# Kernel optimization log

Measured on AMD Instinct MI355X. Metric: run time of the kernel, lower is better.

## Reference

```python
import jax, jax.numpy as jnp
import numpy as np

D_IN, D_OUT, RANK = 4096, 4096, 16
ALPHA = 1.0


def setup_inputs() -> dict:
    key = jax.random.key(0)
    ks = jax.random.split(key, 7)
    x = jax.random.normal(ks[0], (8, 2048, D_IN), dtype=jnp.float32)
    W = jax.random.normal(ks[1], (D_IN, D_OUT), dtype=jnp.float32) * (1.0 / np.sqrt(D_IN))
    bias = jax.random.normal(ks[2], (D_OUT,), dtype=jnp.float32) * 0.02
    # he_normal init for a factors; b factors are zeros in the layer, but use small
    # random values so the adapter path contributes numerically to the test.
    a0 = jax.random.normal(ks[3], (D_IN, RANK), dtype=jnp.float32) * np.sqrt(2.0 / D_IN)
    b0 = jax.random.normal(ks[4], (RANK, D_OUT), dtype=jnp.float32) * 0.02
    a1 = jax.random.normal(ks[5], (D_IN, RANK), dtype=jnp.float32) * np.sqrt(2.0 / D_IN)
    b1 = jax.random.normal(ks[6], (RANK, D_OUT), dtype=jnp.float32) * 0.02
    return {"x": x, "W": W, "bias": bias, "a0": a0, "b0": b0, "a1": a1, "b1": b1}


def reference(x, W, bias, a0, b0, a1, b1):
    # LoHA kernel: base + Hadamard product of scaled low-rank factors
    scale = ALPHA / RANK
    p0 = scale * (a0 @ b0)            # [d_in, d_out]
    p1 = scale * (a1 @ b1)            # [d_in, d_out]
    kernel = W + p0 * p1              # [d_in, d_out]
    # Dense call: x @ kernel + bias
    return jnp.einsum('bsd,de->bse', x, kernel) + bias
```

## Files before the change

kernel.cpp:

```cpp
#include <hip/hip_runtime.h>


#define D_IN   4096
#define D_OUT  4096
#define RANKR  16
#define MROWS  16384
#define NTK    128

typedef __attribute__((ext_vector_type(8))) short short8;
typedef __attribute__((ext_vector_type(4))) float floatx4;

__device__ __forceinline__ unsigned short f2bf(float f) {
    union { float f; unsigned u; } c; c.f = f;
    unsigned r = c.u + 0x7fffu + ((c.u >> 16) & 1u);
    return (unsigned short)(r >> 16);
}

__device__ __forceinline__ void glds16(const void* g, void* l) {
    __builtin_amdgcn_global_load_lds(
        (const __attribute__((address_space(1))) void*)g,
        (__attribute__((address_space(3))) void*)l, 16, 0, 0);
}

__global__ __launch_bounds__(256) void cvt_x(const float* __restrict__ x,
                                             unsigned short* __restrict__ xb) {
    size_t i = ((size_t)blockIdx.x * 256 + threadIdx.x) * 8;
    const float4* p = (const float4*)(x + i);
    float4 v0 = p[0], v1 = p[1];
    union { unsigned short u[8]; uint4 q; } o;
    o.u[0] = f2bf(v0.x); o.u[1] = f2bf(v0.y);
    o.u[2] = f2bf(v0.z); o.u[3] = f2bf(v0.w);
    o.u[4] = f2bf(v1.x); o.u[5] = f2bf(v1.y);
    o.u[6] = f2bf(v1.z); o.u[7] = f2bf(v1.w);
    *(uint4*)(xb + i) = o.q;
}

__global__ __launch_bounds__(256) void prep_bt(
    const float* __restrict__ W,  const float* __restrict__ a0,
    const float* __restrict__ b0, const float* __restrict__ a1,
    const float* __restrict__ b1, unsigned short* __restrict__ Bt) {
    __shared__ float Wt[64][65];
    __shared__ float b0t[64][20], b1t[64][20];
    const int tid = threadIdx.x;
    const int k0 = (blockIdx.x & 63) * 64, n0 = (blockIdx.x >> 6) * 64;

    #pragma unroll
    for (int i = 0; i < 16; ++i) {
        int e = i * 256 + tid;
        int kk = e >> 6, nn = e & 63;
        Wt[kk][nn] = W[(size_t)(k0 + kk) * D_OUT + n0 + nn];
    }
    #pragma unroll
    for (int i = 0; i < 4; ++i) {
        int e = i * 256 + tid;
        int r = e >> 6, nn = e & 63;
        b0t[nn][r] = b0[(size_t)r * D_OUT + n0 + nn];
        b1t[nn][r] = b1[(size_t)r * D_OUT + n0 + nn];
    }
    const int kk = tid & 63;
    float4 A0[4], A1[4];
    #pragma unroll
    for (int c = 0; c < 4; ++c) {
        A0[c] = *(const float4*)(a0 + (size_t)(k0 + kk) * RANKR + c * 4);
        A1[c] = *(const float4*)(a1 + (size_t)(k0 + kk) * RANKR + c * 4);
    }
    __syncthreads();

    const float s2 = 1.0f / 256.0f;
    #pragma unroll
    for (int i = 0; i < 16; ++i) {
        int nn = i * 4 + (tid >> 6);
        float d0 = 0.f, d1 = 0.f;
        #pragma unroll
        for (int c = 0; c < 4; ++c) {
            float4 bv0 = *(const float4*)&b0t[nn][c * 4];
            float4 bv1 = *(const float4*)&b1t[nn][c * 4];
            d0 += A0[c].x * bv0.x + A0[c].y * bv0.y + A0[c].z * bv0.z + A0[c].w * bv0.w;
            d1 += A1[c].x * bv1.x + A1[c].y * bv1.y + A1[c].z * bv1.z + A1[c].w * bv1.w;
        }
        float v = Wt[kk][nn] + s2 * d0 * d1;
        Bt[(size_t)(n0 + nn) * D_IN + k0 + kk] = f2bf(v);
    }
}

#define STAGE_A(tt) do {                                                      \
    const int kt_ = (tt) * 32;                                                \
    unsigned short* const dst_ = &As[(tt) & 3][0];                            \
    _Pragma("unroll")                                                         \
    for (int r_ = 0; r_ < 2; ++r_) {                                          \
      const int e_ = r_ * 512 + tid;                                          \
      const int row_ = e_ >> 2;                                               \
      const int cc_ = ((e_ & 3) ^ ((row_ >> 2) & 3)) * 8;                     \
      glds16(Ag + (size_t)row_ * D_IN + kt_ + cc_,                            \
             (char*)dst_ + r_ * 8192 + wave * 1024);                          \
    }                                                                         \
  } while (0)

#define STAGE_B(tt) do {                                                      \
    const int kt_ = (tt) * 32;                                                \
    unsigned short* const dst_ = &Bs[(tt) & 3][0];                            \
    _Pragma("unroll")                                                         \
    for (int r_ = 0; r_ < 2; ++r_) {                                          \
      const int e_ = r_ * 512 + tid;                                          \
      const int row_ = e_ >> 2;                                               \
      const int cc_ = ((e_ & 3) ^ ((row_ >> 2) & 3)) * 8;                     \
      glds16(Bg + (size_t)row_ * D_IN + kt_ + cc_,                            \
             (char*)dst_ + r_ * 8192 + wave * 1024);                          \
    }                                                                         \
  } while (0)

#define TILE(tt, DS) do {                                                     \
    const unsigned short* const as_ = &As[(tt) & 3][0];                       \
    const unsigned short* const bs_ = &Bs[(tt) & 3][0];                       \
    if (DS) STAGE_A((tt) + 3);                                                \
    short8 bfr[4], afr[4];                                                    \
    _Pragma("unroll")                                                         \
    for (int nt_ = 0; nt_ < 4; ++nt_)                                         \
      bfr[nt_] = *(const short8*)(bs_ + (wn * 64 + nt_ * 16 + l16) * 32 + rc8); \
    _Pragma("unroll")                                                         \
    for (int mt_ = 0; mt_ < 4; ++mt_)                                         \
      afr[mt_] = *(const short8*)(as_ + (wm * 128 + mt_ * 16 + l16) * 32 + rc8); \
    __builtin_amdgcn_s_setprio(1);                                            \
    _Pragma("unroll")                                                         \
    for (int mt_ = 0; mt_ < 4; ++mt_)                                         \
      _Pragma("unroll")                                                       \
      for (int nt_ = 0; nt_ < 4; ++nt_)                                       \
        acc[mt_][nt_] = __builtin_amdgcn_mfma_f32_16x16x32_bf16(              \
            afr[mt_], bfr[nt_], acc[mt_][nt_], 0, 0, 0);                      \
    __builtin_amdgcn_s_setprio(0);                                            \
    if (DS) STAGE_B((tt) + 3);                                                \
    _Pragma("unroll")                                                         \
    for (int mt_ = 0; mt_ < 4; ++mt_)                                         \
      afr[mt_] = *(const short8*)(as_ + (wm * 128 + 64 + mt_ * 16 + l16) * 32 + rc8); \
    __builtin_amdgcn_s_setprio(1);                                            \
    _Pragma("unroll")                                                         \
    for (int mt_ = 0; mt_ < 4; ++mt_)                                         \
      _Pragma("unroll")                                                       \
      for (int nt_ = 0; nt_ < 4; ++nt_)                                       \
        acc[4 + mt_][nt_] = __builtin_amdgcn_mfma_f32_16x16x32_bf16(          \
            afr[mt_], bfr[nt_], acc[4 + mt_][nt_], 0, 0, 0);                  \
    __builtin_amdgcn_s_setprio(0);                                            \
  } while (0)

#define TILE_SYNC(N) do {                                                     \
    asm volatile("s_waitcnt vmcnt(" #N ")" ::: "memory");                     \
    __builtin_amdgcn_s_barrier();                                             \
    asm volatile("" ::: "memory");                                            \
  } while (0)

__global__ __launch_bounds__(512, 2) void gemm_bt(
    const unsigned short* __restrict__ A,
    const unsigned short* __restrict__ B,
    const float* __restrict__ bias,
    float* __restrict__ C) {
    __shared__ __align__(16) unsigned short As[4][256 * 32];
    __shared__ __align__(16) unsigned short Bs[4][256 * 32];

    const int tid  = threadIdx.x;
    const int wave = tid >> 6, lane = tid & 63;
    const int quad = lane >> 4, l16 = lane & 15;
    const int rc8  = (quad ^ (l16 >> 2)) * 8;

    const int bid = blockIdx.y * 16 + blockIdx.x;
    const int swz = (bid & 7) * 128 + (bid >> 3);
    const int m0 = (swz >> 4) * 256, n0 = (swz & 15) * 256;
    const int wm = wave >> 2, wn = wave & 3;

    const unsigned short* Ag = A + (size_t)m0 * D_IN;
    const unsigned short* Bg = B + (size_t)n0 * D_IN;

    floatx4 acc[8][4] = {};

    STAGE_A(0); STAGE_B(0);
    STAGE_A(1); STAGE_B(1);
    STAGE_A(2); STAGE_B(2);
    TILE_SYNC(8);

    for (int t = 0; t < NTK - 3; ++t) {
        TILE(t, 1);
        TILE_SYNC(8);
    }
    TILE(NTK - 3, 0); TILE_SYNC(4);
    TILE(NTK - 2, 0); TILE_SYNC(0);
    TILE(NTK - 1, 0);

    #pragma unroll
    for (int nt = 0; nt < 4; ++nt) {
        int col = n0 + wn * 64 + nt * 16 + l16;
        float bv = bias[col];
        #pragma unroll
        for (int mt = 0; mt < 8; ++mt) {
            int r0 = m0 + wm * 128 + mt * 16 + quad * 4;
            #pragma unroll
            for (int r = 0; r < 4; ++r) {
                float v = acc[mt][nt][r] + bv;
                __builtin_nontemporal_store(v, &C[(size_t)(r0 + r) * D_OUT + col]);
            }
        }
    }
}

extern "C" void kernel_launch(void* const* d_in, const int* in_sizes, int n_in,
                              void* d_out, int out_size, void* d_ws, size_t ws_size,
                              hipStream_t stream) {
    const float* x    = (const float*)d_in[0];
    const float* W    = (const float*)d_in[1];
    const float* bias = (const float*)d_in[2];
    const float* a0   = (const float*)d_in[3];
    const float* b0   = (const float*)d_in[4];
    const float* a1   = (const float*)d_in[5];
    const float* b1   = (const float*)d_in[6];
    float* out = (float*)d_out;

    unsigned short* xb = (unsigned short*)d_ws;
    unsigned short* Bt = (unsigned short*)((char*)d_ws + (size_t)MROWS * D_IN * 2);

    cvt_x<<<(MROWS * (size_t)D_IN) / 2048, 256, 0, stream>>>(x, xb);
    prep_bt<<<4096, 256, 0, stream>>>(W, a0, b0, a1, b1, Bt);
    gemm_bt<<<dim3(D_OUT / 256, MROWS / 256), 512, 0, stream>>>(xb, Bt, bias, out);
}
```

Before: 1.157 ms.

## Restructure GEMM main loop into ping-pong double-buffered 64-wide K tiles

Replaces the 4-stage, 32-wide K pipeline with a 2-buffer scheme where each buffer holds two 32-wide K halves (64 per tile). LDS fragment reads, MFMA blocks and global-to-LDS staging are interleaved at a finer grain, with barriers around each MFMA block and a one-step software lag on the accumulation. The LDS swizzle pattern also changes. The aim is better overlap of LDS reads and memory staging with MFMA work. In exchange it adds many more barriers and more live fragment registers, which could lower occupancy or add stalls.

```diff
diff --git a/kernel.cpp b/kernel.cpp
--- a/kernel.cpp
+++ b/kernel.cpp
@@ -5,7 +5,7 @@
 #define D_OUT  4096
 #define RANKR  16
 #define MROWS  16384
-#define NTK    128
+#define NTILES 64
 
 typedef __attribute__((ext_vector_type(8))) short short8;
 typedef __attribute__((ext_vector_type(4))) float floatx4;
@@ -83,69 +83,50 @@
     }
 }
 
-#define STAGE_A(tt) do {                                                      \
-    const int kt_ = (tt) * 32;                                                \
-    unsigned short* const dst_ = &As[(tt) & 3][0];                            \
-    _Pragma("unroll")                                                         \
-    for (int r_ = 0; r_ < 2; ++r_) {                                          \
-      const int e_ = r_ * 512 + tid;                                          \
-      const int row_ = e_ >> 2;                                               \
-      const int cc_ = ((e_ & 3) ^ ((row_ >> 2) & 3)) * 8;                     \
-      glds16(Ag + (size_t)row_ * D_IN + kt_ + cc_,                            \
-             (char*)dst_ + r_ * 8192 + wave * 1024);                          \
-    }                                                                         \
-  } while (0)
-
-#define STAGE_B(tt) do {                                                      \
-    const int kt_ = (tt) * 32;                                                \
-    unsigned short* const dst_ = &Bs[(tt) & 3][0];                            \
-    _Pragma("unroll")                                                         \
-    for (int r_ = 0; r_ < 2; ++r_) {                                          \
-      const int e_ = r_ * 512 + tid;                                          \
-      const int row_ = e_ >> 2;                                               \
-      const int cc_ = ((e_ & 3) ^ ((row_ >> 2) & 3)) * 8;                     \
-      glds16(Bg + (size_t)row_ * D_IN + kt_ + cc_,                            \
-             (char*)dst_ + r_ * 8192 + wave * 1024);                          \
-    }                                                                         \
-  } while (0)
-
-#define TILE(tt, DS) do {                                                     \
-    const unsigned short* const as_ = &As[(tt) & 3][0];                       \
-    const unsigned short* const bs_ = &Bs[(tt) & 3][0];                       \
-    if (DS) STAGE_A((tt) + 3);                                                \
-    short8 bfr[4], afr[4];                                                    \
-    _Pragma("unroll")                                                         \
-    for (int nt_ = 0; nt_ < 4; ++nt_)                                         \
-      bfr[nt_] = *(const short8*)(bs_ + (wn * 64 + nt_ * 16 + l16) * 32 + rc8); \
-    _Pragma("unroll")                                                         \
-    for (int mt_ = 0; mt_ < 4; ++mt_)                                         \
-      afr[mt_] = *(const short8*)(as_ + (wm * 128 + mt_ * 16 + l16) * 32 + rc8); \
+#define BAR do { asm volatile("" ::: "memory");                  \
+                 __builtin_amdgcn_s_barrier();                   \
+                 asm volatile("" ::: "memory"); } while (0)
+#define VMC(N) asm volatile("s_waitcnt vmcnt(" #N ")" ::: "memory")
+#define LGKM0  asm volatile("s_waitcnt lgkmcnt(0)" ::: "memory")
+
+#define STG_A(NB, KK, KTN) do {                                               \
+    glds16(Ag + gof0 + (KTN) + (KK) * 32, (char*)&As[NB][KK][0] + ldw0);      \
+    glds16(Ag + gof1 + (KTN) + (KK) * 32, (char*)&As[NB][KK][0] + ldw1);      \
+  } while (0)
+#define STG_B(NB, KK, KTN) do {                                               \
+    glds16(Bg + gof0 + (KTN) + (KK) * 32, (char*)&Bs[NB][KK][0] + ldw0);      \
+    glds16(Bg + gof1 + (KTN) + (KK) * 32, (char*)&Bs[NB][KK][0] + ldw1);      \
+  } while (0)
+
+#define RD(DST, SRC, ROWB) _Pragma("unroll")                                  \
+    for (int i_ = 0; i_ < 4; ++i_)                                            \
+      DST[i_] = *(const short8*)(&SRC[((ROWB) + i_ * 16) * 32 + rc8]);
+
+#define MM(AO, AF, BF) do {                                                   \
     __builtin_amdgcn_s_setprio(1);                                            \
     _Pragma("unroll")                                                         \
-    for (int mt_ = 0; mt_ < 4; ++mt_)                                         \
+    for (int i_ = 0; i_ < 4; ++i_)                                            \
       _Pragma("unroll")                                                       \
-      for (int nt_ = 0; nt_ < 4; ++nt_)                                       \
-        acc[mt_][nt_] = __builtin_amdgcn_mfma_f32_16x16x32_bf16(              \
-            afr[mt_], bfr[nt_], acc[mt_][nt_], 0, 0, 0);                      \
+      for (int j_ = 0; j_ < 4; ++j_)                                          \
+        acc[(AO) + i_][j_] = __builtin_amdgcn_mfma_f32_16x16x32_bf16(         \
+            AF[i_], BF[j_], acc[(AO) + i_][j_], 0, 0, 0);                     \
     __builtin_amdgcn_s_setprio(0);                                            \
-    if (DS) STAGE_B((tt) + 3);                                                \
-    _Pragma("unroll")                                                         \
-    for (int mt_ = 0; mt_ < 4; ++mt_)                                         \
-      afr[mt_] = *(const short8*)(as_ + (wm * 128 + 64 + mt_ * 16 + l16) * 32 + rc8); \
-    __builtin_amdgcn_s_setprio(1);                                            \
-    _Pragma("unroll")                                                         \
-    for (int mt_ = 0; mt_ < 4; ++mt_)                                         \
-      _Pragma("unroll")                                                       \
-      for (int nt_ = 0; nt_ < 4; ++nt_)                                       \
-        acc[4 + mt_][nt_] = __builtin_amdgcn_mfma_f32_16x16x32_bf16(          \
-            afr[mt_], bfr[nt_], acc[4 + mt_][nt_], 0, 0, 0);                  \
-    __builtin_amdgcn_s_setprio(0);                                            \
-  } while (0)
-
-#define TILE_SYNC(N) do {                                                     \
-    asm volatile("s_waitcnt vmcnt(" #N ")" ::: "memory");                     \
-    __builtin_amdgcn_s_barrier();                                             \
-    asm volatile("" ::: "memory");                                            \
+  } while (0)
+
+#define TILE(T, BUF) do {                                                     \
+    const int ktn_ = ((T) + 1) * 64;                                          \
+     RD(a0k0, As[BUF][0], arow); RD(b0, Bs[BUF][0], brow);              \
+           STG_A(!(BUF), 0, ktn_);                                            \
+           BAR; LGKM0; MM(4, a1k1, b1); BAR;                                  \
+     RD(a1k0, As[BUF][0], arow + 64);                                   \
+           STG_B(!(BUF), 0, ktn_); VMC(4);                                    \
+           BAR; LGKM0; MM(0, a0k0, b0); BAR;                                  \
+     RD(a0k1, As[BUF][1], arow); RD(b1, Bs[BUF][1], brow);              \
+           STG_A(!(BUF), 1, ktn_);                                            \
+           BAR; LGKM0; MM(4, a1k0, b0); BAR;                                  \
+     RD(a1k1, As[BUF][1], arow + 64);                                   \
+           STG_B(!(BUF), 1, ktn_); VMC(4);                                    \
+           BAR; LGKM0; MM(0, a0k1, b1); BAR;                                  \
   } while (0)
 
 __global__ __launch_bounds__(512, 2) void gemm_bt(
@@ -153,36 +134,62 @@
     const unsigned short* __restrict__ B,
     const float* __restrict__ bias,
     float* __restrict__ C) {
-    __shared__ __align__(16) unsigned short As[4][256 * 32];
-    __shared__ __align__(16) unsigned short Bs[4][256 * 32];
+    __shared__ __align__(16) unsigned short As[2][2][8192];
+    __shared__ __align__(16) unsigned short Bs[2][2][8192];
 
     const int tid  = threadIdx.x;
     const int wave = tid >> 6, lane = tid & 63;
     const int quad = lane >> 4, l16 = lane & 15;
-    const int rc8  = (quad ^ (l16 >> 2)) * 8;
+    const int rc8 = (quad ^ ((l16 >> 1) & 3)) * 8;
 
     const int bid = blockIdx.y * 16 + blockIdx.x;
     const int swz = (bid & 7) * 128 + (bid >> 3);
     const int m0 = (swz >> 4) * 256, n0 = (swz & 15) * 256;
     const int wm = wave >> 2, wn = wave & 3;
+    const int arow = wm * 128 + l16;
+    const int brow = wn * 64 + l16;
 
     const unsigned short* Ag = A + (size_t)m0 * D_IN;
     const unsigned short* Bg = B + (size_t)n0 * D_IN;
 
+    const int e0 = tid, e1 = 512 + tid;
+    const size_t gof0 = (size_t)(e0 >> 2) * D_IN + (size_t)(((e0 & 3) ^ ((e0 >> 3) & 3)) * 8);
+    const size_t gof1 = (size_t)(e1 >> 2) * D_IN + (size_t)(((e1 & 3) ^ ((e1 >> 3) & 3)) * 8);
+    const unsigned ldw0 = wave * 1024;
+    const unsigned ldw1 = 8192 + wave * 1024;
+
+    short8 a0k0[4], a1k0[4], a0k1[4], a1k1[4], b0[4], b1[4];
     floatx4 acc[8][4] = {};
 
-    STAGE_A(0); STAGE_B(0);
-    STAGE_A(1); STAGE_B(1);
-    STAGE_A(2); STAGE_B(2);
-    TILE_SYNC(8);
-
-    for (int t = 0; t < NTK - 3; ++t) {
+    STG_A(0, 0, 0); STG_B(0, 0, 0); STG_A(0, 1, 0); STG_B(0, 1, 0);
+    STG_A(1, 0, 64); STG_B(1, 0, 64);
+    VMC(8);
+    BAR;
+
+     RD(a0k0, As[0][0], arow); RD(b0, Bs[0][0], brow); BAR;
+     RD(a1k0, As[0][0], arow + 64); VMC(4);
+           BAR; LGKM0; MM(0, a0k0, b0); BAR;
+     RD(a0k1, As[0][1], arow); RD(b1, Bs[0][1], brow);
+           STG_A(1, 1, 64);
+           BAR; LGKM0; MM(4, a1k0, b0); BAR;
+     RD(a1k1, As[0][1], arow + 64);
+           STG_B(1, 1, 64); VMC(4);
+           BAR; LGKM0; MM(0, a0k1, b1); BAR;
+
+    for (int t = 1; t < NTILES - 2; t += 2) {
         TILE(t, 1);
-        TILE_SYNC(8);
-    }
-    TILE(NTK - 3, 0); TILE_SYNC(4);
-    TILE(NTK - 2, 0); TILE_SYNC(0);
-    TILE(NTK - 1, 0);
+        TILE(t + 1, 0);
+    }
+
+     RD(a0k0, As[1][0], arow); RD(b0, Bs[1][0], brow);
+           BAR; LGKM0; MM(4, a1k1, b1); BAR;
+     RD(a1k0, As[1][0], arow + 64); VMC(0);
+           BAR; LGKM0; MM(0, a0k0, b0); BAR;
+     RD(a0k1, As[1][1], arow); RD(b1, Bs[1][1], brow);
+           BAR; LGKM0; MM(4, a1k0, b0); BAR;
+     RD(a1k1, As[1][1], arow + 64);
+           BAR; LGKM0; MM(0, a0k1, b1); BAR;
+     MM(4, a1k1, b1);
 
     #pragma unroll
     for (int nt = 0; nt < 4; ++nt) {
```

Result: faster. 1.003 ms (-13.3%).
